# Performance work log

Hardware: AMD Instinct MI355X
Metric: run time of the kernel (lower is better)

## Reference

```python
import jax, jax.numpy as jnp
import numpy as np

G = 2048            # number of graphs in batch
NPG = 128           # nodes per graph (fixed, implied by Linear(128*hid, 1))
IN_C = 151
HID = 64
N = G * NPG
E = 2_097_152       # intra-graph edges, avg degree 8
NEG_SLOPE = 0.2


def setup_inputs() -> dict:
    key = jax.random.key(0)
    ks = jax.random.split(key, 8)
    x = jax.random.normal(ks[0], (N, IN_C), dtype=jnp.float32)
    # intra-graph random edges: pick a graph, then src/dst within it
    g = jax.random.randint(ks[1], (E,), 0, G)
    src = g * NPG + jax.random.randint(ks[2], (E,), 0, NPG)
    dst = g * NPG + jax.random.randint(ks[3], (E,), 0, NPG)
    edge_index = jnp.stack([src, dst]).astype(jnp.int32)   # [2, E]
    W1 = jax.random.normal(ks[4], (IN_C, HID), jnp.float32) / np.sqrt(IN_C)
    att_src = jax.random.normal(ks[5], (HID,), jnp.float32) * 0.1
    att_dst = jax.random.normal(ks[6], (HID,), jnp.float32) * 0.1
    b1 = jnp.zeros((HID,), jnp.float32)
    Wlin = jax.random.normal(ks[7], (NPG * HID, 1), jnp.float32) / np.sqrt(NPG * HID)
    blin = jnp.zeros((1,), jnp.float32)
    return {"x": x, "edge_index": edge_index, "W1": W1, "att_src": att_src,
            "att_dst": att_dst, "b1": b1, "Wlin": Wlin, "blin": blin}


def gat_conv(x, edge_index, W, a_src, a_dst, b):
    """PyG GATConv, heads=1, concat=True, add_self_loops=True."""
    n = x.shape[0]
    h = x @ W                                   # [N, HID] transformed features
    loops = jnp.arange(n, dtype=edge_index.dtype)
    src = jnp.concatenate([edge_index[0], loops])
    dst = jnp.concatenate([edge_index[1], loops])
    # edge score: a_src . h[j] + a_dst . h[i], j->i
    alpha = (h @ a_src)[src] + (h @ a_dst)[dst]            # [E+N]
    alpha = jax.nn.leaky_relu(alpha, NEG_SLOPE)
    # segment softmax over incoming edges of each target node
    amax = jax.ops.segment_max(alpha, dst, num_segments=n)
    ex = jnp.exp(alpha - amax[dst])
    denom = jax.ops.segment_sum(ex, dst, num_segments=n)
    w = ex / denom[dst]                                    # [E+N]
    out = jax.ops.segment_sum(h[src] * w[:, None], dst, num_segments=n)
    return out + b


def reference(x, edge_index, W1, att_src, att_dst, b1, Wlin, blin):
    h = jax.nn.relu(gat_conv(x, edge_index, W1, att_src, att_dst, b1))  # [N, HID]
    h = h.reshape(G, NPG * HID)        # linearize(x, batch): 128 nodes/graph
    logits = h @ Wlin + blin           # [G, 1]
    return jax.nn.sigmoid(logits)
```

## Files before the change

### kernel.cpp

```cpp
#include <hip/hip_runtime.h>
#include <hip/hip_bf16.h>

#define G_ 2048
#define NPG_ 128
#define INC_ 151
#define HID_ 64
#define NNODES_ (G_ * NPG_)
#define NEDGES_ 2097152

typedef __hip_bfloat16 bf16;
typedef short bf16x8v __attribute__((ext_vector_type(8)));
typedef float f32x4 __attribute__((ext_vector_type(4)));

static __device__ __forceinline__ short f2bs(float f) {
    __hip_bfloat16 b = __float2bfloat16(f);
    return __builtin_bit_cast(short, b);
}
static __device__ __forceinline__ float b2f(short s) {
    unsigned int u = ((unsigned int)(unsigned short)s) << 16;
    return __builtin_bit_cast(float, u);
}

__global__ void __launch_bounds__(256) k0C1(const float* __restrict__ W1,
                                            bf16* __restrict__ Bt,
                                            const int* __restrict__ ei,
                                            unsigned int* __restrict__ bccount) {
    __shared__ unsigned int hist[256];
    const int tid = threadIdx.x;
    if (blockIdx.x >= 256) {
        int i = (blockIdx.x - 256) * 256 + tid;
        if (i < 64 * 168) {
            int n = i / 168, k = i - n * 168;
            float v = (k < 151) ? W1[k * 64 + n] : 0.f;
            Bt[i] = __float2bfloat16(v);
        }
        return;
    }
    hist[tid] = 0;
    __syncthreads();
    const int e0 = blockIdx.x * 8192;
    for (int e = e0 + tid; e < e0 + 8192; e += 256)
        atomicAdd(&hist[ei[e] >> 10], 1u);
    __syncthreads();
    bccount[blockIdx.x * 256 + tid] = hist[tid];
}

__global__ void __launch_bounds__(256) k1_mfma(
        const float* __restrict__ x, const bf16* __restrict__ Bt,
        const float* __restrict__ att_src, const float* __restrict__ att_dst,
        bf16* __restrict__ h, float* __restrict__ as_, float* __restrict__ ad_) {
    __shared__ __align__(16) bf16 Bs[64 * 168];
    const int tid = threadIdx.x;
    const int rowbase = blockIdx.x * 64;

    {
        const uint4* s = (const uint4*)Bt;
        uint4* d = (uint4*)Bs;
        for (int i = tid; i < 1344; i += 256) d[i] = s[i];
    }
    __syncthreads();

    const int wv = tid >> 6, lane = tid & 63;
    const int quad = lane >> 4, m = lane & 15;
    const int row = rowbase + wv * 16 + m;
    const float* xr = x + (size_t)row * 151;

    f32x4 acc[4];
#pragma unroll
    for (int t = 0; t < 4; t++) acc[t] = (f32x4){0.f, 0.f, 0.f, 0.f};

#pragma unroll
    for (int ks = 0; ks < 5; ks++) {
        const int k0 = ks * 32 + quad * 8;
        float a[8];
        if (ks < 4) {
#pragma unroll
            for (int e = 0; e < 8; e++) a[e] = xr[k0 + e];
        } else {
#pragma unroll
            for (int e = 0; e < 8; e++) {
                int c = k0 + e;
                a[e] = (c < 151) ? xr[c] : 0.f;
            }
        }
        bf16x8v af = {f2bs(a[0]), f2bs(a[1]), f2bs(a[2]), f2bs(a[3]),
                      f2bs(a[4]), f2bs(a[5]), f2bs(a[6]), f2bs(a[7])};
#pragma unroll
        for (int t = 0; t < 4; t++) {
            bf16x8v bfr = *(const bf16x8v*)&Bs[(t * 16 + m) * 168 + k0];
            acc[t] = __builtin_amdgcn_mfma_f32_16x16x32_bf16(af, bfr, acc[t], 0, 0, 0);
        }
    }

    float as4[4], ad4[4];
#pragma unroll
    for (int t = 0; t < 4; t++) {
        as4[t] = att_src[t * 16 + m];
        ad4[t] = att_dst[t * 16 + m];
    }
#pragma unroll
    for (int r = 0; r < 4; r++) {
        float s = acc[0][r] * as4[0] + acc[1][r] * as4[1] +
                  acc[2][r] * as4[2] + acc[3][r] * as4[3];
        float d = acc[0][r] * ad4[0] + acc[1][r] * ad4[1] +
                  acc[2][r] * ad4[2] + acc[3][r] * ad4[3];
#pragma unroll
        for (int off = 1; off <= 8; off <<= 1) {
            s += __shfl_xor(s, off);
            d += __shfl_xor(d, off);
        }
        const int node = rowbase + wv * 16 + quad * 4 + r;
        if (m == 0) { as_[node] = s; ad_[node] = d; }
#pragma unroll
        for (int t = 0; t < 4; t++) {
            float val = acc[t][r];
            float oth = __shfl_xor(val, 1);
            if (!(lane & 1)) {
                unsigned short lo = (unsigned short)f2bs(val);
                unsigned short hi = (unsigned short)f2bs(oth);
                unsigned int u = ((unsigned int)hi << 16) | lo;
                *(unsigned int*)&h[(size_t)node * 64 + t * 16 + m] = u;
            }
        }
    }
}

__global__ void __launch_bounds__(256) kC2a(unsigned int* __restrict__ bccount,
                                            unsigned int* __restrict__ totals) {
    __shared__ unsigned int sc[256];
    const int tid = threadIdx.x, bk = blockIdx.x;
    unsigned int c = bccount[tid * 256 + bk];
    sc[tid] = c;
    __syncthreads();
    for (int off = 1; off < 256; off <<= 1) {
        unsigned int v = (tid >= off) ? sc[tid - off] : 0;
        __syncthreads();
        sc[tid] += v;
        __syncthreads();
    }
    bccount[tid * 256 + bk] = sc[tid] - c;
    if (tid == 255) totals[bk] = sc[255];
}

__global__ void __launch_bounds__(256) kC2b(const unsigned int* __restrict__ totals,
                                            unsigned int* __restrict__ cbase,
                                            unsigned int* __restrict__ base4) {
    __shared__ unsigned int sc[256];
    const int tid = threadIdx.x;
    unsigned int c = totals[tid];
    sc[tid] = c;
    __syncthreads();
    for (int off = 1; off < 256; off <<= 1) {
        unsigned int v = (tid >= off) ? sc[tid - off] : 0;
        __syncthreads();
        sc[tid] += v;
        __syncthreads();
    }
    cbase[tid] = sc[tid] - c;
    if (tid == 255) {
        cbase[256] = sc[255];
        base4[G_ * 4] = NEDGES_;
    }
}

__global__ void __launch_bounds__(256) kC3_scatter(const int* __restrict__ ei,
                                                   const unsigned int* __restrict__ bccount,
                                                   const unsigned int* __restrict__ cbase,
                                                   unsigned int* __restrict__ rbuf) {
    __shared__ unsigned int cur[256];
    const int tid = threadIdx.x;
    cur[tid] = cbase[tid] + bccount[blockIdx.x * 256 + tid];
    __syncthreads();
    const int e0 = blockIdx.x * 8192;
    for (int e = e0 + tid; e < e0 + 8192; e += 256) {
        int s = ei[e];
        int d = ei[NEDGES_ + e];
        int bk = s >> 10;
        unsigned int pos = atomicAdd(&cur[bk], 1u);
        rbuf[pos] = (((unsigned int)s & 1023u) << 7) | ((unsigned int)d & 127u);
    }
}

__global__ void __launch_bounds__(256) kC4_fine(const unsigned int* __restrict__ rbuf,
                                                const unsigned int* __restrict__ cbase,
                                                unsigned int* __restrict__ base4,
                                                unsigned short* __restrict__ eb) {
    __shared__ unsigned int lcnt[32];
    __shared__ unsigned int cur[32];
    const int tid = threadIdx.x;
    const int b = blockIdx.x;
    const unsigned int s0 = cbase[b], s1 = cbase[b + 1];
    if (tid < 32) lcnt[tid] = 0;
    __syncthreads();
    for (unsigned int i = s0 + tid; i < s1; i += 256) {
        unsigned int rec = rbuf[i];
        int key = ((rec >> 12) & 0x1C) | ((rec >> 5) & 3);
        atomicAdd(&lcnt[key], 1u);
    }
    __syncthreads();
    if (tid == 0) {
        unsigned int r = 0;
#pragma unroll
        for (int j = 0; j < 32; j++) {
            base4[b * 32 + j] = s0 + r;
            cur[j] = s0 + r;
            r += lcnt[j];
        }
    }
    __syncthreads();
    const int lane = tid & 63;
    for (unsigned int i = s0 + tid; i < s1; i += 256) {
        unsigned int rec = rbuf[i];
        int key = ((rec >> 12) & 0x1C) | ((rec >> 5) & 3);
        unsigned long long m = __ballot(1);
#pragma unroll
        for (int bit = 0; bit < 5; bit++) {
            unsigned long long bb = __ballot((key >> bit) & 1);
            m &= ((key >> bit) & 1) ? bb : ~bb;
        }
        int leader = __builtin_ctzll(m);
        int rank = __builtin_popcountll(m & ((1ull << lane) - 1ull));
        unsigned int bp = 0;
        if (lane == leader)
            bp = atomicAdd(&cur[key], (unsigned int)__builtin_popcountll(m));
        bp = __shfl((int)bp, leader);
        eb[bp + rank] = (unsigned short)(rec & 0x3FFFu);
    }
}

__global__ void __launch_bounds__(256) k3_graph(
        const unsigned short* __restrict__ eb, const unsigned int* __restrict__ base4,
        const bf16* __restrict__ h,
        const float* __restrict__ as_, const float* __restrict__ ad_,
        const float* __restrict__ b1, const float* __restrict__ Wlin,
        const float* __restrict__ blin, float* __restrict__ out) {
    __shared__ __align__(16) unsigned char lds[52736];
    short* Ab = (short*)lds;
    float* S = (float*)(lds + 34816);
    short* hT = (short*)(lds + 34816);
    float* dinv = (float*)(lds + 52224);

    const int tid = threadIdx.x;
    const int g = blockIdx.x;
    const float* asg = as_ + (g << 7);
    const float* adg = ad_ + (g << 7);
    const unsigned int* hgu = (const unsigned int*)(h + ((size_t)g << 13));

#pragma unroll 1
    for (int p = 0; p < 4; p++) {
        for (int i = tid; i < 1024; i += 256)
            ((float4*)S)[i] = make_float4(0.f, 0.f, 0.f, 0.f);
        __syncthreads();
        if (tid < 32) {
            int node = 32 * p + tid;
            float a = asg[node] + adg[node];
            a = (a > 0.f) ? a : 0.2f * a;
            atomicAdd(&S[(tid << 7) + node], __expf(a));
        }
        const unsigned int q0 = base4[(g << 2) + p];
        const unsigned int q1 = base4[(g << 2) + p + 1];
        for (unsigned int k = q0 + tid; k < q1; k += 256) {
            unsigned int v = eb[k];
            int sl = v >> 7, dl = v & 127;
            float a = asg[sl] + adg[dl];
            a = (a > 0.f) ? a : 0.2f * a;
            atomicAdd(&S[((dl & 31) << 7) + sl], __expf(a));
        }
        __syncthreads();
        float rs[2];
#pragma unroll
        for (int hf = 0; hf < 2; hf++) {
            int c = tid + (hf << 8);
            int r = c >> 4;
            int col = (c & 15) << 3;
            float4 v0 = ((const float4*)S)[c * 2];
            float4 v1 = ((const float4*)S)[c * 2 + 1];
            rs[hf] = v0.x + v0.y + v0.z + v0.w + v1.x + v1.y + v1.z + v1.w;
            bf16x8v pk = {f2bs(v0.x), f2bs(v0.y), f2bs(v0.z), f2bs(v0.w),
                          f2bs(v1.x), f2bs(v1.y), f2bs(v1.z), f2bs(v1.w)};
            *(bf16x8v*)&Ab[(32 * p + r) * 136 + col] = pk;
        }
#pragma unroll
        for (int off = 1; off <= 8; off <<= 1) {
            rs[0] += __shfl_xor(rs[0], off);
            rs[1] += __shfl_xor(rs[1], off);
        }
        if ((tid & 15) == 0) {
            dinv[32 * p + (tid >> 4)] = 1.f / rs[0];
            dinv[32 * p + 16 + (tid >> 4)] = 1.f / rs[1];
        }
        __syncthreads();
    }

    for (int idx = tid; idx < 4096; idx += 256) {
        unsigned int u = hgu[idx];
        int j = idx >> 5, f2 = idx & 31;
        hT[(2 * f2) * 136 + j] = (short)(u & 0xFFFF);
        hT[(2 * f2 + 1) * 136 + j] = (short)(u >> 16);
    }
    __syncthreads();

    const int w = tid >> 6, lane = tid & 63;
    const int quad = lane >> 4, m = lane & 15;
    const int i0 = w * 32;
    f32x4 acc[2][4];
#pragma unroll
    for (int mt = 0; mt < 2; mt++)
#pragma unroll
        for (int nt = 0; nt < 4; nt++) acc[mt][nt] = (f32x4){0.f, 0.f, 0.f, 0.f};

#pragma unroll
    for (int ks = 0; ks < 4; ks++) {
        const int k0 = ks * 32 + quad * 8;
        bf16x8v a0 = *(const bf16x8v*)&Ab[(i0 + m) * 136 + k0];
        bf16x8v a1 = *(const bf16x8v*)&Ab[(i0 + 16 + m) * 136 + k0];
#pragma unroll
        for (int nt = 0; nt < 4; nt++) {
            bf16x8v bfr = *(const bf16x8v*)&hT[(nt * 16 + m) * 136 + k0];
            acc[0][nt] = __builtin_amdgcn_mfma_f32_16x16x32_bf16(a0, bfr, acc[0][nt], 0, 0, 0);
            acc[1][nt] = __builtin_amdgcn_mfma_f32_16x16x32_bf16(a1, bfr, acc[1][nt], 0, 0, 0);
        }
    }

    float dv[2][4];
#pragma unroll
    for (int mt = 0; mt < 2; mt++)
#pragma unroll
        for (int r = 0; r < 4; r++)
            dv[mt][r] = dinv[i0 + mt * 16 + quad * 4 + r];

    float p = 0.f;
#pragma unroll
    for (int nt = 0; nt < 4; nt++) {
        float bb = b1[nt * 16 + m];
#pragma unroll
        for (int mt = 0; mt < 2; mt++) {
#pragma unroll
            for (int r = 0; r < 4; r++) {
                int il = i0 + mt * 16 + quad * 4 + r;
                float v = acc[mt][nt][r] * dv[mt][r] + bb;
                v = v > 0.f ? v : 0.f;
                p += v * Wlin[il * 64 + nt * 16 + m];
            }
        }
    }
#pragma unroll
    for (int off = 32; off; off >>= 1) p += __shfl_xor(p, off);

    __syncthreads();
    if (lane == 0) S[w] = p;
    __syncthreads();
    if (tid == 0) {
        float logit = S[0] + S[1] + S[2] + S[3] + blin[0];
        out[g] = 1.f / (1.f + __expf(-logit));
    }
}

extern "C" void kernel_launch(void* const* d_in, const int* in_sizes, int n_in,
                              void* d_out, int out_size, void* d_ws, size_t ws_size,
                              hipStream_t stream) {
    (void)in_sizes; (void)n_in; (void)out_size; (void)ws_size;
    const float* x       = (const float*)d_in[0];
    const int*   ei      = (const int*)d_in[1];
    const float* W1      = (const float*)d_in[2];
    const float* att_src = (const float*)d_in[3];
    const float* att_dst = (const float*)d_in[4];
    const float* b1      = (const float*)d_in[5];
    const float* Wlin    = (const float*)d_in[6];
    const float* blin    = (const float*)d_in[7];
    float* out = (float*)d_out;

    char* ws = (char*)d_ws;
    bf16*           h       = (bf16*)ws;
    float*          as_     = (float*)(ws + 33554432);
    float*          ad_     = (float*)(ws + 34603008);
    bf16*           Bt      = (bf16*)(ws + 35651584);
    unsigned int*   bccount = (unsigned int*)(ws + 35717120);
    unsigned int*   cbase   = (unsigned int*)(ws + 35979264);
    unsigned int*   totals  = (unsigned int*)(ws + 35983360);
    unsigned int*   base4   = (unsigned int*)(ws + 35987456);
    unsigned int*   rbuf    = (unsigned int*)(ws + 36024320);
    unsigned short* eb      = (unsigned short*)(ws + 44412928);

    k0C1<<<298, 256, 0, stream>>>(W1, Bt, ei, bccount);
    k1_mfma<<<NNODES_ / 64, 256, 0, stream>>>(x, Bt, att_src, att_dst, h, as_, ad_);
    kC2a<<<256, 256, 0, stream>>>(bccount, totals);
    kC2b<<<1, 256, 0, stream>>>(totals, cbase, base4);
    kC3_scatter<<<256, 256, 0, stream>>>(ei, bccount, cbase, rbuf);
    kC4_fine<<<256, 256, 0, stream>>>(rbuf, cbase, base4, eb);
    k3_graph<<<G_, 256, 0, stream>>>(eb, base4, h, as_, ad_, b1, Wlin, blin, out);
}
```

Before: 370.3 us.

## Replace multi-pass counting sort with single-pass fixed-slot bucket scatter

Swaps the histogram, two prefix-scan kernels, coarse scatter and fine sort for one kernel that appends each edge into a fixed 512-slot bucket per (graph, dst-quarter), using global atomic counters. Edges past a bucket's capacity go to a small overflow list, which the graph kernel scans linearly. This removes four kernel launches and a full intermediate pass over the edges, at the cost of global atomic contention and a memset. Correctness needs the overflow to stay under its 4096 cap. Bucket occupancy is about 256 on average, so overflow should be rare.

```diff
diff --git a/kernel.cpp b/kernel.cpp
--- a/kernel.cpp
+++ b/kernel.cpp
@@ -7,6 +7,8 @@
 #define HID_ 64
 #define NNODES_ (G_ * NPG_)
 #define NEDGES_ 2097152
+#define SLOTS_ 512
+#define OVFCAP_ 4096
 
 typedef __hip_bfloat16 bf16;
 typedef short bf16x8v __attribute__((ext_vector_type(8)));
@@ -16,33 +18,36 @@
     __hip_bfloat16 b = __float2bfloat16(f);
     return __builtin_bit_cast(short, b);
 }
-static __device__ __forceinline__ float b2f(short s) {
-    unsigned int u = ((unsigned int)(unsigned short)s) << 16;
-    return __builtin_bit_cast(float, u);
-}
-
-__global__ void __launch_bounds__(256) k0C1(const float* __restrict__ W1,
-                                            bf16* __restrict__ Bt,
-                                            const int* __restrict__ ei,
-                                            unsigned int* __restrict__ bccount) {
-    __shared__ unsigned int hist[256];
+
+__global__ void __launch_bounds__(256) kS_scatter(const int* __restrict__ ei,
+                                                  unsigned int* __restrict__ gcount,
+                                                  unsigned int* __restrict__ ovfcnt,
+                                                  unsigned int* __restrict__ ovf,
+                                                  unsigned short* __restrict__ eb,
+                                                  const float* __restrict__ W1,
+                                                  bf16* __restrict__ Bt) {
     const int tid = threadIdx.x;
     if (blockIdx.x >= 256) {
         int i = (blockIdx.x - 256) * 256 + tid;
-        if (i < 64 * 168) {
-            int n = i / 168, k = i - n * 168;
-            float v = (k < 151) ? W1[k * 64 + n] : 0.f;
-            Bt[i] = __float2bfloat16(v);
-        }
+        int n = i / 168, k = i - n * 168;
+        float v = (k < 151) ? W1[k * 64 + n] : 0.f;
+        Bt[i] = __float2bfloat16(v);
         return;
     }
-    hist[tid] = 0;
-    __syncthreads();
     const int e0 = blockIdx.x * 8192;
-    for (int e = e0 + tid; e < e0 + 8192; e += 256)
-        atomicAdd(&hist[ei[e] >> 10], 1u);
-    __syncthreads();
-    bccount[blockIdx.x * 256 + tid] = hist[tid];
+    for (int e = e0 + tid; e < e0 + 8192; e += 256) {
+        int s = ei[e];
+        int d = ei[NEDGES_ + e];
+        unsigned int key = (((unsigned int)s >> 7) << 2) | (((unsigned int)d >> 5) & 3u);
+        unsigned int rec = (((unsigned int)s & 127u) << 7) | ((unsigned int)d & 127u);
+        unsigned int pos = atomicAdd(&gcount[key], 1u);
+        if (pos < SLOTS_) {
+            eb[(key << 9) + pos] = (unsigned short)rec;
+        } else {
+            unsigned int oi = atomicAdd(ovfcnt, 1u);
+            if (oi < OVFCAP_) ovf[oi] = (key << 14) | rec;
+        }
+    }
 }
 
 __global__ void __launch_bounds__(256) k1_mfma(
@@ -125,111 +130,9 @@
     }
 }
 
-__global__ void __launch_bounds__(256) kC2a(unsigned int* __restrict__ bccount,
-                                            unsigned int* __restrict__ totals) {
-    __shared__ unsigned int sc[256];
-    const int tid = threadIdx.x, bk = blockIdx.x;
-    unsigned int c = bccount[tid * 256 + bk];
-    sc[tid] = c;
-    __syncthreads();
-    for (int off = 1; off < 256; off <<= 1) {
-        unsigned int v = (tid >= off) ? sc[tid - off] : 0;
-        __syncthreads();
-        sc[tid] += v;
-        __syncthreads();
-    }
-    bccount[tid * 256 + bk] = sc[tid] - c;
-    if (tid == 255) totals[bk] = sc[255];
-}
-
-__global__ void __launch_bounds__(256) kC2b(const unsigned int* __restrict__ totals,
-                                            unsigned int* __restrict__ cbase,
-                                            unsigned int* __restrict__ base4) {
-    __shared__ unsigned int sc[256];
-    const int tid = threadIdx.x;
-    unsigned int c = totals[tid];
-    sc[tid] = c;
-    __syncthreads();
-    for (int off = 1; off < 256; off <<= 1) {
-        unsigned int v = (tid >= off) ? sc[tid - off] : 0;
-        __syncthreads();
-        sc[tid] += v;
-        __syncthreads();
-    }
-    cbase[tid] = sc[tid] - c;
-    if (tid == 255) {
-        cbase[256] = sc[255];
-        base4[G_ * 4] = NEDGES_;
-    }
-}
-
-__global__ void __launch_bounds__(256) kC3_scatter(const int* __restrict__ ei,
-                                                   const unsigned int* __restrict__ bccount,
-                                                   const unsigned int* __restrict__ cbase,
-                                                   unsigned int* __restrict__ rbuf) {
-    __shared__ unsigned int cur[256];
-    const int tid = threadIdx.x;
-    cur[tid] = cbase[tid] + bccount[blockIdx.x * 256 + tid];
-    __syncthreads();
-    const int e0 = blockIdx.x * 8192;
-    for (int e = e0 + tid; e < e0 + 8192; e += 256) {
-        int s = ei[e];
-        int d = ei[NEDGES_ + e];
-        int bk = s >> 10;
-        unsigned int pos = atomicAdd(&cur[bk], 1u);
-        rbuf[pos] = (((unsigned int)s & 1023u) << 7) | ((unsigned int)d & 127u);
-    }
-}
-
-__global__ void __launch_bounds__(256) kC4_fine(const unsigned int* __restrict__ rbuf,
-                                                const unsigned int* __restrict__ cbase,
-                                                unsigned int* __restrict__ base4,
-                                                unsigned short* __restrict__ eb) {
-    __shared__ unsigned int lcnt[32];
-    __shared__ unsigned int cur[32];
-    const int tid = threadIdx.x;
-    const int b = blockIdx.x;
-    const unsigned int s0 = cbase[b], s1 = cbase[b + 1];
-    if (tid < 32) lcnt[tid] = 0;
-    __syncthreads();
-    for (unsigned int i = s0 + tid; i < s1; i += 256) {
-        unsigned int rec = rbuf[i];
-        int key = ((rec >> 12) & 0x1C) | ((rec >> 5) & 3);
-        atomicAdd(&lcnt[key], 1u);
-    }
-    __syncthreads();
-    if (tid == 0) {
-        unsigned int r = 0;
-#pragma unroll
-        for (int j = 0; j < 32; j++) {
-            base4[b * 32 + j] = s0 + r;
-            cur[j] = s0 + r;
-            r += lcnt[j];
-        }
-    }
-    __syncthreads();
-    const int lane = tid & 63;
-    for (unsigned int i = s0 + tid; i < s1; i += 256) {
-        unsigned int rec = rbuf[i];
-        int key = ((rec >> 12) & 0x1C) | ((rec >> 5) & 3);
-        unsigned long long m = __ballot(1);
-#pragma unroll
-        for (int bit = 0; bit < 5; bit++) {
-            unsigned long long bb = __ballot((key >> bit) & 1);
-            m &= ((key >> bit) & 1) ? bb : ~bb;
-        }
-        int leader = __builtin_ctzll(m);
-        int rank = __builtin_popcountll(m & ((1ull << lane) - 1ull));
-        unsigned int bp = 0;
-        if (lane == leader)
-            bp = atomicAdd(&cur[key], (unsigned int)__builtin_popcountll(m));
-        bp = __shfl((int)bp, leader);
-        eb[bp + rank] = (unsigned short)(rec & 0x3FFFu);
-    }
-}
-
 __global__ void __launch_bounds__(256) k3_graph(
-        const unsigned short* __restrict__ eb, const unsigned int* __restrict__ base4,
+        const unsigned short* __restrict__ eb, const unsigned int* __restrict__ gcount,
+        const unsigned int* __restrict__ ovfcnt, const unsigned int* __restrict__ ovf,
         const bf16* __restrict__ h,
         const float* __restrict__ as_, const float* __restrict__ ad_,
         const float* __restrict__ b1, const float* __restrict__ Wlin,
@@ -245,6 +148,7 @@
     const float* asg = as_ + (g << 7);
     const float* adg = ad_ + (g << 7);
     const unsigned int* hgu = (const unsigned int*)(h + ((size_t)g << 13));
+    const unsigned int novf = *ovfcnt;
 
 #pragma unroll 1
     for (int p = 0; p < 4; p++) {
@@ -257,14 +161,27 @@
             a = (a > 0.f) ? a : 0.2f * a;
             atomicAdd(&S[(tid << 7) + node], __expf(a));
         }
-        const unsigned int q0 = base4[(g << 2) + p];
-        const unsigned int q1 = base4[(g << 2) + p + 1];
-        for (unsigned int k = q0 + tid; k < q1; k += 256) {
+        const unsigned int key = (g << 2) + p;
+        unsigned int cnt = gcount[key];
+        if (cnt > SLOTS_) cnt = SLOTS_;
+        const unsigned int q0 = key << 9;
+        for (unsigned int k = q0 + tid; k < q0 + cnt; k += 256) {
             unsigned int v = eb[k];
             int sl = v >> 7, dl = v & 127;
             float a = asg[sl] + adg[dl];
             a = (a > 0.f) ? a : 0.2f * a;
             atomicAdd(&S[((dl & 31) << 7) + sl], __expf(a));
+        }
+        if (novf) {
+            for (unsigned int i = tid; i < novf && i < OVFCAP_; i += 256) {
+                unsigned int r = ovf[i];
+                if ((r >> 14) == key) {
+                    int sl = (r >> 7) & 127, dl = r & 127;
+                    float a = asg[sl] + adg[dl];
+                    a = (a > 0.f) ? a : 0.2f * a;
+                    atomicAdd(&S[((dl & 31) << 7) + sl], __expf(a));
+                }
+            }
         }
         __syncthreads();
         float rs[2];
@@ -375,18 +292,13 @@
     float*          as_     = (float*)(ws + 33554432);
     float*          ad_     = (float*)(ws + 34603008);
     bf16*           Bt      = (bf16*)(ws + 35651584);
-    unsigned int*   bccount = (unsigned int*)(ws + 35717120);
-    unsigned int*   cbase   = (unsigned int*)(ws + 35979264);
-    unsigned int*   totals  = (unsigned int*)(ws + 35983360);
-    unsigned int*   base4   = (unsigned int*)(ws + 35987456);
-    unsigned int*   rbuf    = (unsigned int*)(ws + 36024320);
-    unsigned short* eb      = (unsigned short*)(ws + 44412928);
-
-    k0C1<<<298, 256, 0, stream>>>(W1, Bt, ei, bccount);
+    unsigned int*   gcount  = (unsigned int*)(ws + 35717120);
+    unsigned int*   ovfcnt  = (unsigned int*)(ws + 35749888);
+    unsigned int*   ovf     = (unsigned int*)(ws + 35753984);
+    unsigned short* eb      = (unsigned short*)(ws + 35770368);
+
+    hipMemsetAsync(gcount, 0, 36864, stream);
+    kS_scatter<<<298, 256, 0, stream>>>(ei, gcount, ovfcnt, ovf, eb, W1, Bt);
     k1_mfma<<<NNODES_ / 64, 256, 0, stream>>>(x, Bt, att_src, att_dst, h, as_, ad_);
-    kC2a<<<256, 256, 0, stream>>>(bccount, totals);
-    kC2b<<<1, 256, 0, stream>>>(totals, cbase, base4);
-    kC3_scatter<<<256, 256, 0, stream>>>(ei, bccount, cbase, rbuf);
-    kC4_fine<<<256, 256, 0, stream>>>(rbuf, cbase, base4, eb);
-    k3_graph<<<G_, 256, 0, stream>>>(eb, base4, h, as_, ad_, b1, Wlin, blin, out);
-}
+    k3_graph<<<G_, 256, 0, stream>>>(eb, gcount, ovfcnt, ovf, h, as_, ad_, b1, Wlin, blin, out);
+}
```

Result: slower. 385.9 us (+4.2%).

## Merge preprocessing kernels and fold prefix scans into scatter and fine-sort kernels

Applied to the files above, without the earlier changes.

Folds the edge histogram and the W1 transpose/convert into the MFMA projection kernel, so each projection block builds its bf16 weight tile directly in shared memory. The two separate scan kernels are removed, and the scatter and fine-bucket kernels each recompute the needed prefix sums by reading the full 256x256 count table. In the graph kernel, the score matrix is zeroed once up front and then re-zeroed as it is read, instead of with a separate clear loop and barrier per pass. This cuts four kernel launches and their serialization points, at the cost of redundant count-table reads in every scatter/fine block and a per-block W1 transpose across 4096 projection blocks.

```diff
diff --git a/kernel.cpp b/kernel.cpp
--- a/kernel.cpp
+++ b/kernel.cpp
@@ -16,50 +16,36 @@
     __hip_bfloat16 b = __float2bfloat16(f);
     return __builtin_bit_cast(short, b);
 }
-static __device__ __forceinline__ float b2f(short s) {
-    unsigned int u = ((unsigned int)(unsigned short)s) << 16;
-    return __builtin_bit_cast(float, u);
-}
-
-__global__ void __launch_bounds__(256) k0C1(const float* __restrict__ W1,
-                                            bf16* __restrict__ Bt,
-                                            const int* __restrict__ ei,
-                                            unsigned int* __restrict__ bccount) {
-    __shared__ unsigned int hist[256];
-    const int tid = threadIdx.x;
-    if (blockIdx.x >= 256) {
-        int i = (blockIdx.x - 256) * 256 + tid;
-        if (i < 64 * 168) {
-            int n = i / 168, k = i - n * 168;
-            float v = (k < 151) ? W1[k * 64 + n] : 0.f;
-            Bt[i] = __float2bfloat16(v);
-        }
-        return;
-    }
-    hist[tid] = 0;
-    __syncthreads();
-    const int e0 = blockIdx.x * 8192;
-    for (int e = e0 + tid; e < e0 + 8192; e += 256)
-        atomicAdd(&hist[ei[e] >> 10], 1u);
-    __syncthreads();
-    bccount[blockIdx.x * 256 + tid] = hist[tid];
-}
-
-__global__ void __launch_bounds__(256) k1_mfma(
-        const float* __restrict__ x, const bf16* __restrict__ Bt,
+
+__global__ void __launch_bounds__(256) k1x(
+        const float* __restrict__ x, const float* __restrict__ W1,
+        const int* __restrict__ ei, unsigned int* __restrict__ bccount,
         const float* __restrict__ att_src, const float* __restrict__ att_dst,
         bf16* __restrict__ h, float* __restrict__ as_, float* __restrict__ ad_) {
-    __shared__ __align__(16) bf16 Bs[64 * 168];
+    __shared__ __align__(16) unsigned char smem[21504];
     const int tid = threadIdx.x;
-    const int rowbase = blockIdx.x * 64;
-
-    {
-        const uint4* s = (const uint4*)Bt;
-        uint4* d = (uint4*)Bs;
-        for (int i = tid; i < 1344; i += 256) d[i] = s[i];
-    }
-    __syncthreads();
-
+
+    if (blockIdx.x < 256) {
+        unsigned int* hist = (unsigned int*)smem;
+        hist[tid] = 0;
+        __syncthreads();
+        const int e0 = blockIdx.x * 8192;
+        for (int e = e0 + tid; e < e0 + 8192; e += 256)
+            atomicAdd(&hist[ei[e] >> 10], 1u);
+        __syncthreads();
+        bccount[blockIdx.x * 256 + tid] = hist[tid];
+        return;
+    }
+
+    bf16* Bs = (bf16*)smem;
+    for (int i = tid; i < 64 * 168; i += 256) {
+        int n = i / 168, k = i - n * 168;
+        float v = (k < 151) ? W1[k * 64 + n] : 0.f;
+        Bs[i] = __float2bfloat16(v);
+    }
+    __syncthreads();
+
+    const int rowbase = (blockIdx.x - 256) * 64;
     const int wv = tid >> 6, lane = tid & 63;
     const int quad = lane >> 4, m = lane & 15;
     const int row = rowbase + wv * 16 + m;
@@ -125,12 +111,20 @@
     }
 }
 
-__global__ void __launch_bounds__(256) kC2a(unsigned int* __restrict__ bccount,
-                                            unsigned int* __restrict__ totals) {
+__global__ void __launch_bounds__(256) kC3_scatter(const int* __restrict__ ei,
+                                                   const unsigned int* __restrict__ bccount,
+                                                   unsigned int* __restrict__ rbuf) {
     __shared__ unsigned int sc[256];
-    const int tid = threadIdx.x, bk = blockIdx.x;
-    unsigned int c = bccount[tid * 256 + bk];
-    sc[tid] = c;
+    __shared__ unsigned int cur[256];
+    const int tid = threadIdx.x;
+    const int j = blockIdx.x;
+    unsigned int part = 0, tot = 0;
+    for (int i = 0; i < 256; i++) {
+        unsigned int c = bccount[i * 256 + tid];
+        if (i < j) part += c;
+        tot += c;
+    }
+    sc[tid] = tot;
     __syncthreads();
     for (int off = 1; off < 256; off <<= 1) {
         unsigned int v = (tid >= off) ? sc[tid - off] : 0;
@@ -138,40 +132,9 @@
         sc[tid] += v;
         __syncthreads();
     }
-    bccount[tid * 256 + bk] = sc[tid] - c;
-    if (tid == 255) totals[bk] = sc[255];
-}
-
-__global__ void __launch_bounds__(256) kC2b(const unsigned int* __restrict__ totals,
-                                            unsigned int* __restrict__ cbase,
-                                            unsigned int* __restrict__ base4) {
-    __shared__ unsigned int sc[256];
-    const int tid = threadIdx.x;
-    unsigned int c = totals[tid];
-    sc[tid] = c;
-    __syncthreads();
-    for (int off = 1; off < 256; off <<= 1) {
-        unsigned int v = (tid >= off) ? sc[tid - off] : 0;
-        __syncthreads();
-        sc[tid] += v;
-        __syncthreads();
-    }
-    cbase[tid] = sc[tid] - c;
-    if (tid == 255) {
-        cbase[256] = sc[255];
-        base4[G_ * 4] = NEDGES_;
-    }
-}
-
-__global__ void __launch_bounds__(256) kC3_scatter(const int* __restrict__ ei,
-                                                   const unsigned int* __restrict__ bccount,
-                                                   const unsigned int* __restrict__ cbase,
-                                                   unsigned int* __restrict__ rbuf) {
-    __shared__ unsigned int cur[256];
-    const int tid = threadIdx.x;
-    cur[tid] = cbase[tid] + bccount[blockIdx.x * 256 + tid];
-    __syncthreads();
-    const int e0 = blockIdx.x * 8192;
+    cur[tid] = (sc[tid] - tot) + part;
+    __syncthreads();
+    const int e0 = j * 8192;
     for (int e = e0 + tid; e < e0 + 8192; e += 256) {
         int s = ei[e];
         int d = ei[NEDGES_ + e];
@@ -182,16 +145,27 @@
 }
 
 __global__ void __launch_bounds__(256) kC4_fine(const unsigned int* __restrict__ rbuf,
-                                                const unsigned int* __restrict__ cbase,
+                                                const unsigned int* __restrict__ bccount,
                                                 unsigned int* __restrict__ base4,
                                                 unsigned short* __restrict__ eb) {
+    __shared__ unsigned int sc[256];
     __shared__ unsigned int lcnt[32];
     __shared__ unsigned int cur[32];
     const int tid = threadIdx.x;
     const int b = blockIdx.x;
-    const unsigned int s0 = cbase[b], s1 = cbase[b + 1];
+    unsigned int tot = 0;
+    for (int i = 0; i < 256; i++) tot += bccount[i * 256 + tid];
+    sc[tid] = tot;
     if (tid < 32) lcnt[tid] = 0;
     __syncthreads();
+    for (int off = 1; off < 256; off <<= 1) {
+        unsigned int v = (tid >= off) ? sc[tid - off] : 0;
+        __syncthreads();
+        sc[tid] += v;
+        __syncthreads();
+    }
+    const unsigned int s0 = (b > 0) ? sc[b - 1] : 0;
+    const unsigned int s1 = sc[b];
     for (unsigned int i = s0 + tid; i < s1; i += 256) {
         unsigned int rec = rbuf[i];
         int key = ((rec >> 12) & 0x1C) | ((rec >> 5) & 3);
@@ -201,11 +175,12 @@
     if (tid == 0) {
         unsigned int r = 0;
 #pragma unroll
-        for (int j = 0; j < 32; j++) {
-            base4[b * 32 + j] = s0 + r;
-            cur[j] = s0 + r;
-            r += lcnt[j];
-        }
+        for (int jj = 0; jj < 32; jj++) {
+            base4[b * 32 + jj] = s0 + r;
+            cur[jj] = s0 + r;
+            r += lcnt[jj];
+        }
+        if (b == 255) base4[G_ * 4] = NEDGES_;
     }
     __syncthreads();
     const int lane = tid & 63;
@@ -246,11 +221,12 @@
     const float* adg = ad_ + (g << 7);
     const unsigned int* hgu = (const unsigned int*)(h + ((size_t)g << 13));
 
+    const float4 z4 = make_float4(0.f, 0.f, 0.f, 0.f);
+    for (int i = tid; i < 1024; i += 256) ((float4*)S)[i] = z4;
+    __syncthreads();
+
 #pragma unroll 1
     for (int p = 0; p < 4; p++) {
-        for (int i = tid; i < 1024; i += 256)
-            ((float4*)S)[i] = make_float4(0.f, 0.f, 0.f, 0.f);
-        __syncthreads();
         if (tid < 32) {
             int node = 32 * p + tid;
             float a = asg[node] + adg[node];
@@ -275,6 +251,8 @@
             int col = (c & 15) << 3;
             float4 v0 = ((const float4*)S)[c * 2];
             float4 v1 = ((const float4*)S)[c * 2 + 1];
+            ((float4*)S)[c * 2] = z4;
+            ((float4*)S)[c * 2 + 1] = z4;
             rs[hf] = v0.x + v0.y + v0.z + v0.w + v1.x + v1.y + v1.z + v1.w;
             bf16x8v pk = {f2bs(v0.x), f2bs(v0.y), f2bs(v0.z), f2bs(v0.w),
                           f2bs(v1.x), f2bs(v1.y), f2bs(v1.z), f2bs(v1.w)};
@@ -374,19 +352,13 @@
     bf16*           h       = (bf16*)ws;
     float*          as_     = (float*)(ws + 33554432);
     float*          ad_     = (float*)(ws + 34603008);
-    bf16*           Bt      = (bf16*)(ws + 35651584);
-    unsigned int*   bccount = (unsigned int*)(ws + 35717120);
-    unsigned int*   cbase   = (unsigned int*)(ws + 35979264);
-    unsigned int*   totals  = (unsigned int*)(ws + 35983360);
-    unsigned int*   base4   = (unsigned int*)(ws + 35987456);
-    unsigned int*   rbuf    = (unsigned int*)(ws + 36024320);
-    unsigned short* eb      = (unsigned short*)(ws + 44412928);
-
-    k0C1<<<298, 256, 0, stream>>>(W1, Bt, ei, bccount);
-    k1_mfma<<<NNODES_ / 64, 256, 0, stream>>>(x, Bt, att_src, att_dst, h, as_, ad_);
-    kC2a<<<256, 256, 0, stream>>>(bccount, totals);
-    kC2b<<<1, 256, 0, stream>>>(totals, cbase, base4);
-    kC3_scatter<<<256, 256, 0, stream>>>(ei, bccount, cbase, rbuf);
-    kC4_fine<<<256, 256, 0, stream>>>(rbuf, cbase, base4, eb);
+    unsigned int*   bccount = (unsigned int*)(ws + 35651584);
+    unsigned int*   base4   = (unsigned int*)(ws + 35913728);
+    unsigned int*   rbuf    = (unsigned int*)(ws + 35950592);
+    unsigned short* eb      = (unsigned short*)(ws + 44339200);
+
+    k1x<<<4352, 256, 0, stream>>>(x, W1, ei, bccount, att_src, att_dst, h, as_, ad_);
+    kC3_scatter<<<256, 256, 0, stream>>>(ei, bccount, rbuf);
+    kC4_fine<<<256, 256, 0, stream>>>(rbuf, bccount, base4, eb);
     k3_graph<<<G_, 256, 0, stream>>>(eb, base4, h, as_, ad_, b1, Wlin, blin, out);
 }
```

Measured after the change: 429.1 us. 1.16x slower.
